# Performance work log

Hardware: AMD Instinct MI355X
Metric: run time of the kernel (lower is better)

Reference implementation:

```python
import jax, jax.numpy as jnp
import numpy as np

CLASSES = [20, 70, 250, 800, 3000, 12000]
DIM = 768
B = 2048


def setup_inputs() -> dict:
    key = jax.random.key(0)
    ks = jax.random.split(key, 2 * len(CLASSES) + 1)
    inp = {"x": jax.random.normal(ks[0], (B, DIM), jnp.float32)}
    scale = 1.0 / np.sqrt(DIM).astype(np.float32)
    for i, c in enumerate(CLASSES):
        # Concatenation of all per-node generator Linear layers at level i.
        inp[f"W{i}"] = jax.random.normal(ks[1 + i], (c, DIM), jnp.float32) * scale
        inp[f"b{i}"] = jnp.zeros((c,), jnp.float32)
    for lvl in range(1, 6):
        k = jax.random.fold_in(key, 100 + lvl)
        # parent index (at level lvl-1) of each class at level lvl; sorted -> contiguous sibling groups
        inp[f"p{lvl}"] = jnp.sort(
            jax.random.randint(k, (CLASSES[lvl],), 0, CLASSES[lvl - 1], jnp.int32)
        )
    return inp


def _segment_softmax_cols(logits, parent, num_parents):
    """Softmax over columns of logits [B, C], within groups of columns sharing a parent."""
    lt = logits.T  # [C, B]
    mx = jax.ops.segment_max(lt, parent, num_segments=num_parents)  # [P, B]
    e = jnp.exp(lt - mx[parent])
    s = jax.ops.segment_sum(e, parent, num_segments=num_parents)  # [P, B]
    return (e / s[parent]).T  # [B, C]


def reference(x, W0, b0, W1, b1, W2, b2, W3, b3, W4, b4, W5, b5, p1, p2, p3, p4, p5):
    # Level 0: root generator = Linear + Softmax over all level-0 classes.
    out = jax.nn.softmax(x @ W0.T + b0, axis=1)  # [B, classes[0]]
    outputs = [out]
    Ws = [W1, W2, W3, W4, W5]
    bs = [b1, b2, b3, b4, b5]
    ps = [p1, p2, p3, p4, p5]
    for lvl in range(5):
        logits = x @ Ws[lvl].T + bs[lvl]  # [B, classes[lvl+1]]
        cond = _segment_softmax_cols(logits, ps[lvl], CLASSES[lvl])  # per-parent softmax
        out = cond * outputs[-1][:, ps[lvl]]  # scatter of prob * subtree(x) == gather of parent prob
        outputs.append(out)
    return tuple(outputs)
```

## Files before the change

### kernel.cpp

```cpp
#include <hip/hip_runtime.h>
#include <stdint.h>

#define BDIM 2048
#define KDIM 768
#define NTOT 16140
#define NKT 24

typedef _Float16 half8 __attribute__((ext_vector_type(8)));
typedef float floatx4 __attribute__((ext_vector_type(4)));

__device__ __forceinline__ unsigned short f2h(float f) {
  _Float16 h = (_Float16)f;
  return __builtin_bit_cast(unsigned short, h);
}

__device__ __forceinline__ void level_of(int col, int& cb, int& Cl, long long& ob) {
  if      (col < 20)   { cb = 0;    Cl = 20;    ob = 0LL; }
  else if (col < 90)   { cb = 20;   Cl = 70;    ob = 40960LL; }
  else if (col < 340)  { cb = 90;   Cl = 250;   ob = 184320LL; }
  else if (col < 1140) { cb = 340;  Cl = 800;   ob = 696320LL; }
  else if (col < 4140) { cb = 1140; Cl = 3000;  ob = 2334720LL; }
  else                 { cb = 4140; Cl = 12000; ob = 8478720LL; }
}

__device__ __forceinline__ void gload_lds16(const void* g, void* l) {
  __builtin_amdgcn_global_load_lds(
      (const __attribute__((address_space(1))) unsigned int*)g,
      (__attribute__((address_space(3))) unsigned int*)l, 16, 0, 0);
}

__global__ __launch_bounds__(256) void convert_kernel(
    const float* __restrict__ x,
    const float* __restrict__ W0, const float* __restrict__ W1,
    const float* __restrict__ W2, const float* __restrict__ W3,
    const float* __restrict__ W4, const float* __restrict__ W5,
    unsigned short* __restrict__ xh, unsigned short* __restrict__ wh)
{
  long long i4 = (long long)blockIdx.x * 256 + threadIdx.x;
  if (i4 >= 3492096LL) return;
  long long e = i4 * 4;
  const long long XN = (long long)BDIM * KDIM;
  float4 v;
  unsigned short* dst;
  if (e < XN) {
    v = reinterpret_cast<const float4*>(x)[i4];
    dst = xh + e;
  } else {
    long long we = e - XN;
    const float* src; long long off;
    if      (we < 15360)    { src = W0; off = we; }
    else if (we < 69120)    { src = W1; off = we - 15360; }
    else if (we < 261120)   { src = W2; off = we - 69120; }
    else if (we < 875520)   { src = W3; off = we - 261120; }
    else if (we < 3179520)  { src = W4; off = we - 875520; }
    else                    { src = W5; off = we - 3179520; }
    v = reinterpret_cast<const float4*>(src)[off >> 2];
    dst = wh + we;
  }
  ushort4 o;
  o.x = f2h(v.x); o.y = f2h(v.y); o.z = f2h(v.z); o.w = f2h(v.w);
  *reinterpret_cast<ushort4*>(dst) = o;
}

__global__ __launch_bounds__(256) void seg_build_kernel(
    const int* __restrict__ p1, const int* __restrict__ p2, const int* __restrict__ p3,
    const int* __restrict__ p4, const int* __restrict__ p5, int* __restrict__ seg)
{
  int idx = blockIdx.x * 256 + threadIdx.x;
  if (idx >= 4147) return;
  int L, s;
  if      (idx < 2)    { L = 0; s = idx; }
  else if (idx < 23)   { L = 1; s = idx - 2; }
  else if (idx < 94)   { L = 2; s = idx - 23; }
  else if (idx < 345)  { L = 3; s = idx - 94; }
  else if (idx < 1146) { L = 4; s = idx - 345; }
  else                 { L = 5; s = idx - 1146; }
  int val;
  if (L == 0) {
    val = (s == 0) ? 0 : 20;
  } else {
    const int* p = (L == 1) ? p1 : (L == 2) ? p2 : (L == 3) ? p3 : (L == 4) ? p4 : p5;
    int C = (L == 1) ? 70 : (L == 2) ? 250 : (L == 3) ? 800 : (L == 4) ? 3000 : 12000;
    int lo = 0, hi = C;
    while (lo < hi) { int mid = (lo + hi) >> 1; if (p[mid] < s) lo = mid + 1; else hi = mid; }
    val = lo;
  }
  seg[idx] = val;
}

#define EPI_STRIDE 132

__global__ __launch_bounds__(256, 2) void gemm_kernel(
    const unsigned short* __restrict__ Ah,
    const unsigned short* __restrict__ Wh,
    float* __restrict__ out)
{
  __shared__ __align__(16) char smem_raw[64 * EPI_STRIDE * 4];
  float* epi = (float*)smem_raw;

  const int bid = blockIdx.x;
  const int logical = (bid & 7) * 254 + (bid >> 3);
  const int cx = logical >> 4;
  const int row0 = (logical & 15) * 128;
  const int col0 = cx * 128;

  const int tid  = threadIdx.x;
  const int wave = tid >> 6;
  const int lane = tid & 63;
  const int wr = (wave >> 1) * 64;
  const int wc = (wave & 1) * 64;
  const int q  = lane >> 4;
  const int lr = lane & 15;

  const int rquad = lane >> 2;
  const int kq = lane & 3;

  floatx4 acc[4][4];
#pragma unroll
  for (int i = 0; i < 4; ++i)
#pragma unroll
    for (int j = 0; j < 4; ++j)
      acc[i][j] = (floatx4){0.f, 0.f, 0.f, 0.f};

  const unsigned short* gA[2];
  const unsigned short* gB[2];
#pragma unroll
  for (int i = 0; i < 2; ++i) {
    int c = 2 * wave + i;
    int rowA = row0 + 16 * c + rquad;
    gA[i] = Ah + (long long)rowA * KDIM + kq * 8;
    int colB = col0 + 16 * c + rquad;
    if (colB >= NTOT) colB = NTOT - 1;
    gB[i] = Wh + (long long)colB * KDIM + kq * 8;
  }

  auto stage = [&](int buf, int kt) {
#pragma unroll
    for (int i = 0; i < 2; ++i) {
      int c = 2 * wave + i;
      gload_lds16(gA[i] + kt * 32, smem_raw + buf * 8192 + c * 1024);
      gload_lds16(gB[i] + kt * 32, smem_raw + 16384 + buf * 8192 + c * 1024);
    }
  };

  int cur = 0;
  stage(0, 0);
  __syncthreads();

  for (int kt = 0; kt < NKT; ++kt) {
    if (kt + 1 < NKT) stage(cur ^ 1, kt + 1);
    const char* Ac = smem_raw + cur * 8192;
    const char* Bc = smem_raw + 16384 + cur * 8192;
    half8 af[4], bf[4];
#pragma unroll
    for (int i = 0; i < 4; ++i)
      af[i] = __builtin_bit_cast(half8, *(const uint4*)(Ac + (wr + i * 16 + lr) * 64 + q * 16));
#pragma unroll
    for (int j = 0; j < 4; ++j)
      bf[j] = __builtin_bit_cast(half8, *(const uint4*)(Bc + (wc + j * 16 + lr) * 64 + q * 16));
#pragma unroll
    for (int i = 0; i < 4; ++i)
#pragma unroll
      for (int j = 0; j < 4; ++j)
        acc[i][j] = __builtin_amdgcn_mfma_f32_16x16x32_f16(af[i], bf[j], acc[i][j], 0, 0, 0);
    __syncthreads();
    cur ^= 1;
  }

  int cbA, ClA; long long obA; level_of(col0, cbA, ClA, obA);
  int cbB, ClB; long long obB; level_of(col0 + 127, cbB, ClB, obB);
  const bool fast = (cbA == cbB) && ((cbA & 3) == 0) && ((ClA & 3) == 0) && (col0 + 128 <= NTOT);

  for (int h = 0; h < 2; ++h) {
    __syncthreads();
    if ((wave >> 1) == h) {
#pragma unroll
      for (int i = 0; i < 4; ++i)
#pragma unroll
        for (int j = 0; j < 4; ++j)
#pragma unroll
          for (int rg = 0; rg < 4; ++rg)
            epi[(i * 16 + q * 4 + rg) * EPI_STRIDE + wc + j * 16 + lr] = acc[i][j][rg];
    }
    __syncthreads();
    if (fast) {
      const long long rowbase = obA + (long long)(row0 + h * 64) * ClA + (col0 - cbA);
#pragma unroll
      for (int it = 0; it < 8; ++it) {
        int idx = it * 256 + tid;
        int r = idx >> 5, f4 = idx & 31;
        float4 v = *(const float4*)(epi + r * EPI_STRIDE + f4 * 4);
        *(float4*)(out + rowbase + (long long)r * ClA + f4 * 4) = v;
      }
    } else {
      for (int idx = tid; idx < 64 * 128; idx += 256) {
        int r = idx >> 7, c = idx & 127;
        int col = col0 + c;
        if (col < NTOT) {
          int cb, Cl; long long ob; level_of(col, cb, Cl, ob);
          out[ob + (long long)(row0 + h * 64 + r) * Cl + (col - cb)] = epi[r * EPI_STRIDE + c];
        }
      }
    }
  }
}

__global__ __launch_bounds__(512) void tree_softmax_kernel(
    float* __restrict__ out,
    const float* __restrict__ b0, const float* __restrict__ b1, const float* __restrict__ b2,
    const float* __restrict__ b3, const float* __restrict__ b4, const float* __restrict__ b5,
    const int* __restrict__ seg,
    const int* __restrict__ p1, const int* __restrict__ p2, const int* __restrict__ p3,
    const int* __restrict__ p4, const int* __restrict__ p5)
{
  __shared__ __align__(16) float l[NTOT];
  __shared__ float rs[3000];
  const int tid = threadIdx.x;
  const int row = blockIdx.x;
  const float* bias[6] = {b0, b1, b2, b3, b4, b5};
  const int* par[6] = {nullptr, p1, p2, p3, p4, p5};
  const int Cn[6] = {20, 70, 250, 800, 3000, 12000};
  const int Pn[6] = {1, 20, 70, 250, 800, 3000};
  const int lb[6] = {0, 20, 90, 340, 1140, 4140};
  const int so[6] = {0, 2, 23, 94, 345, 1146};
  const long long ob[6] = {0, 40960, 184320, 696320, 2334720, 8478720};

#pragma unroll
  for (int L = 0; L < 6; ++L) {
    const float* src = out + ob[L] + (long long)row * Cn[L];
    const float* bs = bias[L];
    float* dst = l + lb[L];
    if ((Cn[L] & 3) == 0 && (lb[L] & 3) == 0) {
      const int n4 = Cn[L] >> 2;
      for (int i = tid; i < n4; i += 512) {
        float4 v = reinterpret_cast<const float4*>(src)[i];
        float4 b = reinterpret_cast<const float4*>(bs)[i];
        float4 e;
        e.x = __expf(v.x + b.x); e.y = __expf(v.y + b.y);
        e.z = __expf(v.z + b.z); e.w = __expf(v.w + b.w);
        reinterpret_cast<float4*>(dst)[i] = e;
      }
    } else {
      for (int c = tid; c < Cn[L]; c += 512) dst[c] = __expf(src[c] + bs[c]);
    }
  }
  __syncthreads();

#pragma unroll
  for (int L = 0; L < 6; ++L) {
    const int* sg = seg + so[L];
    float* lv = l + lb[L];
    const float* pv = l + ((L == 0) ? 0 : lb[L - 1]);
    for (int s = tid; s < Pn[L]; s += 512) {
      int st = sg[s], en = sg[s + 1];
      float sum = 0.f;
      for (int c = st; c < en; ++c) sum += lv[c];
      float pp = (L == 0) ? 1.0f : pv[s];
      rs[s] = pp / sum;
    }
    __syncthreads();
    float* dstg = out + ob[L] + (long long)row * Cn[L];
    if (L == 0) {
      float r0 = rs[0];
      for (int c = tid; c < 20; c += 512) { float v = lv[c] * r0; lv[c] = v; dstg[c] = v; }
    } else if ((Cn[L] & 3) == 0 && (lb[L] & 3) == 0) {
      const int* pa = par[L];
      const int n4 = Cn[L] >> 2;
      for (int i = tid; i < n4; i += 512) {
        int4 pi = reinterpret_cast<const int4*>(pa)[i];
        float4 v = reinterpret_cast<const float4*>(lv)[i];
        v.x *= rs[pi.x]; v.y *= rs[pi.y]; v.z *= rs[pi.z]; v.w *= rs[pi.w];
        if (L != 5) reinterpret_cast<float4*>(lv)[i] = v;
        reinterpret_cast<float4*>(dstg)[i] = v;
      }
    } else {
      const int* pa = par[L];
      for (int c = tid; c < Cn[L]; c += 512) {
        float v = lv[c] * rs[pa[c]];
        lv[c] = v; dstg[c] = v;
      }
    }
    __syncthreads();
  }
}

extern "C" void kernel_launch(void* const* d_in, const int* in_sizes, int n_in,
                              void* d_out, int out_size, void* d_ws, size_t ws_size,
                              hipStream_t stream)
{
  const float* x = (const float*)d_in[0];
  const float* W[6]    = {(const float*)d_in[1], (const float*)d_in[3], (const float*)d_in[5],
                          (const float*)d_in[7], (const float*)d_in[9], (const float*)d_in[11]};
  const float* bias[6] = {(const float*)d_in[2], (const float*)d_in[4], (const float*)d_in[6],
                          (const float*)d_in[8], (const float*)d_in[10], (const float*)d_in[12]};
  const int* p[5] = {(const int*)d_in[13], (const int*)d_in[14], (const int*)d_in[15],
                     (const int*)d_in[16], (const int*)d_in[17]};
  float* out = (float*)d_out;
  char* ws = (char*)d_ws;
  unsigned short* xh = (unsigned short*)ws;
  unsigned short* wh = (unsigned short*)(ws + 3145728);
  int* seg = (int*)(ws + 27936768);

  convert_kernel<<<13641, 256, 0, stream>>>(x, W[0], W[1], W[2], W[3], W[4], W[5], xh, wh);
  seg_build_kernel<<<17, 256, 0, stream>>>(p[0], p[1], p[2], p[3], p[4], seg);
  gemm_kernel<<<2032, 256, 0, stream>>>(xh, wh, out);
  tree_softmax_kernel<<<2048, 512, 0, stream>>>(
      out, bias[0], bias[1], bias[2], bias[3], bias[4], bias[5], seg,
      p[0], p[1], p[2], p[3], p[4]);
}
```

Measured before the change: 367.2 us.

## Replace segment-offset tree softmax with LDS atomic sums and register-held leaves

Measured after the change: 454.4 us. 23.8% more time.

```diff
diff --git a/kernel.cpp b/kernel.cpp
--- a/kernel.cpp
+++ b/kernel.cpp
@@ -62,32 +62,6 @@
   *reinterpret_cast<ushort4*>(dst) = o;
 }
 
-__global__ __launch_bounds__(256) void seg_build_kernel(
-    const int* __restrict__ p1, const int* __restrict__ p2, const int* __restrict__ p3,
-    const int* __restrict__ p4, const int* __restrict__ p5, int* __restrict__ seg)
-{
-  int idx = blockIdx.x * 256 + threadIdx.x;
-  if (idx >= 4147) return;
-  int L, s;
-  if      (idx < 2)    { L = 0; s = idx; }
-  else if (idx < 23)   { L = 1; s = idx - 2; }
-  else if (idx < 94)   { L = 2; s = idx - 23; }
-  else if (idx < 345)  { L = 3; s = idx - 94; }
-  else if (idx < 1146) { L = 4; s = idx - 345; }
-  else                 { L = 5; s = idx - 1146; }
-  int val;
-  if (L == 0) {
-    val = (s == 0) ? 0 : 20;
-  } else {
-    const int* p = (L == 1) ? p1 : (L == 2) ? p2 : (L == 3) ? p3 : (L == 4) ? p4 : p5;
-    int C = (L == 1) ? 70 : (L == 2) ? 250 : (L == 3) ? 800 : (L == 4) ? 3000 : 12000;
-    int lo = 0, hi = C;
-    while (lo < hi) { int mid = (lo + hi) >> 1; if (p[mid] < s) lo = mid + 1; else hi = mid; }
-    val = lo;
-  }
-  seg[idx] = val;
-}
-
 #define EPI_STRIDE 132
 
 __global__ __launch_bounds__(256, 2) void gemm_kernel(
@@ -205,82 +179,121 @@
   }
 }
 
-__global__ __launch_bounds__(512) void tree_softmax_kernel(
+__global__ __launch_bounds__(512, 6) void tree_softmax_kernel(
     float* __restrict__ out,
     const float* __restrict__ b0, const float* __restrict__ b1, const float* __restrict__ b2,
     const float* __restrict__ b3, const float* __restrict__ b4, const float* __restrict__ b5,
-    const int* __restrict__ seg,
     const int* __restrict__ p1, const int* __restrict__ p2, const int* __restrict__ p3,
     const int* __restrict__ p4, const int* __restrict__ p5)
 {
-  __shared__ __align__(16) float l[NTOT];
-  __shared__ float rs[3000];
+  __shared__ float e04[4140];
+  __shared__ float S[4141];
   const int tid = threadIdx.x;
-  const int row = blockIdx.x;
-  const float* bias[6] = {b0, b1, b2, b3, b4, b5};
-  const int* par[6] = {nullptr, p1, p2, p3, p4, p5};
-  const int Cn[6] = {20, 70, 250, 800, 3000, 12000};
-  const int Pn[6] = {1, 20, 70, 250, 800, 3000};
-  const int lb[6] = {0, 20, 90, 340, 1140, 4140};
-  const int so[6] = {0, 2, 23, 94, 345, 1146};
-  const long long ob[6] = {0, 40960, 184320, 696320, 2334720, 8478720};
-
-#pragma unroll
-  for (int L = 0; L < 6; ++L) {
-    const float* src = out + ob[L] + (long long)row * Cn[L];
-    const float* bs = bias[L];
-    float* dst = l + lb[L];
-    if ((Cn[L] & 3) == 0 && (lb[L] & 3) == 0) {
-      const int n4 = Cn[L] >> 2;
-      for (int i = tid; i < n4; i += 512) {
-        float4 v = reinterpret_cast<const float4*>(src)[i];
-        float4 b = reinterpret_cast<const float4*>(bs)[i];
-        float4 e;
-        e.x = __expf(v.x + b.x); e.y = __expf(v.y + b.y);
-        e.z = __expf(v.z + b.z); e.w = __expf(v.w + b.w);
-        reinterpret_cast<float4*>(dst)[i] = e;
-      }
-    } else {
-      for (int c = tid; c < Cn[L]; c += 512) dst[c] = __expf(src[c] + bs[c]);
-    }
-  }
-  __syncthreads();
-
-#pragma unroll
-  for (int L = 0; L < 6; ++L) {
-    const int* sg = seg + so[L];
-    float* lv = l + lb[L];
-    const float* pv = l + ((L == 0) ? 0 : lb[L - 1]);
-    for (int s = tid; s < Pn[L]; s += 512) {
-      int st = sg[s], en = sg[s + 1];
-      float sum = 0.f;
-      for (int c = st; c < en; ++c) sum += lv[c];
-      float pp = (L == 0) ? 1.0f : pv[s];
-      rs[s] = pp / sum;
-    }
-    __syncthreads();
-    float* dstg = out + ob[L] + (long long)row * Cn[L];
-    if (L == 0) {
-      float r0 = rs[0];
-      for (int c = tid; c < 20; c += 512) { float v = lv[c] * r0; lv[c] = v; dstg[c] = v; }
-    } else if ((Cn[L] & 3) == 0 && (lb[L] & 3) == 0) {
-      const int* pa = par[L];
-      const int n4 = Cn[L] >> 2;
-      for (int i = tid; i < n4; i += 512) {
-        int4 pi = reinterpret_cast<const int4*>(pa)[i];
-        float4 v = reinterpret_cast<const float4*>(lv)[i];
-        v.x *= rs[pi.x]; v.y *= rs[pi.y]; v.z *= rs[pi.z]; v.w *= rs[pi.w];
-        if (L != 5) reinterpret_cast<float4*>(lv)[i] = v;
-        reinterpret_cast<float4*>(dstg)[i] = v;
-      }
-    } else {
-      const int* pa = par[L];
-      for (int c = tid; c < Cn[L]; c += 512) {
-        float v = lv[c] * rs[pa[c]];
-        lv[c] = v; dstg[c] = v;
-      }
-    }
-    __syncthreads();
+  const long long row = blockIdx.x;
+
+  for (int i = tid; i < 4141; i += 512) S[i] = 0.f;
+  __syncthreads();
+
+  if (tid < 20) {
+    float e = __expf(out[row * 20 + tid] + b0[tid]);
+    e04[tid] = e;
+    atomicAdd(&S[0], e);
+  }
+  if (tid < 70) {
+    float e = __expf(out[40960 + row * 70 + tid] + b1[tid]);
+    e04[20 + tid] = e;
+    atomicAdd(&S[1 + p1[tid]], e);
+  }
+  if (tid < 250) {
+    float e = __expf(out[184320 + row * 250 + tid] + b2[tid]);
+    e04[90 + tid] = e;
+    atomicAdd(&S[21 + p2[tid]], e);
+  }
+  if (tid < 200) {
+    float4 v = reinterpret_cast<const float4*>(out + 696320 + row * 800)[tid];
+    float4 b = reinterpret_cast<const float4*>(b3)[tid];
+    int4  p = reinterpret_cast<const int4*>(p3)[tid];
+    float4 e;
+    e.x = __expf(v.x + b.x); e.y = __expf(v.y + b.y);
+    e.z = __expf(v.z + b.z); e.w = __expf(v.w + b.w);
+    reinterpret_cast<float4*>(e04 + 340)[tid] = e;
+    atomicAdd(&S[91 + p.x], e.x); atomicAdd(&S[91 + p.y], e.y);
+    atomicAdd(&S[91 + p.z], e.z); atomicAdd(&S[91 + p.w], e.w);
+  }
+  for (int i4 = tid; i4 < 750; i4 += 512) {
+    float4 v = reinterpret_cast<const float4*>(out + 2334720 + row * 3000)[i4];
+    float4 b = reinterpret_cast<const float4*>(b4)[i4];
+    int4  p = reinterpret_cast<const int4*>(p4)[i4];
+    float4 e;
+    e.x = __expf(v.x + b.x); e.y = __expf(v.y + b.y);
+    e.z = __expf(v.z + b.z); e.w = __expf(v.w + b.w);
+    reinterpret_cast<float4*>(e04 + 1140)[i4] = e;
+    atomicAdd(&S[341 + p.x], e.x); atomicAdd(&S[341 + p.y], e.y);
+    atomicAdd(&S[341 + p.z], e.z); atomicAdd(&S[341 + p.w], e.w);
+  }
+  float4 e5[6];
+  const float4* l5 = reinterpret_cast<const float4*>(out + 8478720 + row * 12000);
+  const float4* b5v = reinterpret_cast<const float4*>(b5);
+  const int4*  p5v = reinterpret_cast<const int4*>(p5);
+#pragma unroll
+  for (int i = 0; i < 6; ++i) {
+    int i4 = i * 512 + tid;
+    if (i4 < 3000) {
+      float4 v = l5[i4]; float4 b = b5v[i4]; int4 p = p5v[i4];
+      float4 e;
+      e.x = __expf(v.x + b.x); e.y = __expf(v.y + b.y);
+      e.z = __expf(v.z + b.z); e.w = __expf(v.w + b.w);
+      e5[i] = e;
+      atomicAdd(&S[1141 + p.x], e.x); atomicAdd(&S[1141 + p.y], e.y);
+      atomicAdd(&S[1141 + p.z], e.z); atomicAdd(&S[1141 + p.w], e.w);
+    }
+  }
+  __syncthreads();
+
+  if (tid == 0) S[0] = 1.f / S[0];
+  __syncthreads();
+  if (tid < 20)  S[1 + tid]  = e04[tid]       * S[0]            / S[1 + tid];
+  __syncthreads();
+  if (tid < 70)  S[21 + tid] = e04[20 + tid]  * S[1 + p1[tid]]  / S[21 + tid];
+  __syncthreads();
+  if (tid < 250) S[91 + tid] = e04[90 + tid]  * S[21 + p2[tid]] / S[91 + tid];
+  __syncthreads();
+  for (int s = tid; s < 800; s += 512)
+    S[341 + s]  = e04[340 + s]  * S[91 + p3[s]]  / S[341 + s];
+  __syncthreads();
+  for (int s = tid; s < 3000; s += 512)
+    S[1141 + s] = e04[1140 + s] * S[341 + p4[s]] / S[1141 + s];
+  __syncthreads();
+
+  if (tid < 20)
+    out[row * 20 + tid] = e04[tid] * S[0];
+  if (tid < 70)
+    out[40960 + row * 70 + tid] = e04[20 + tid] * S[1 + p1[tid]];
+  if (tid < 250)
+    out[184320 + row * 250 + tid] = e04[90 + tid] * S[21 + p2[tid]];
+  if (tid < 200) {
+    int4 p = reinterpret_cast<const int4*>(p3)[tid];
+    float4 e = reinterpret_cast<const float4*>(e04 + 340)[tid];
+    e.x *= S[91 + p.x]; e.y *= S[91 + p.y]; e.z *= S[91 + p.z]; e.w *= S[91 + p.w];
+    reinterpret_cast<float4*>(out + 696320 + row * 800)[tid] = e;
+  }
+  for (int i4 = tid; i4 < 750; i4 += 512) {
+    int4 p = reinterpret_cast<const int4*>(p4)[i4];
+    float4 e = reinterpret_cast<const float4*>(e04 + 1140)[i4];
+    e.x *= S[341 + p.x]; e.y *= S[341 + p.y]; e.z *= S[341 + p.z]; e.w *= S[341 + p.w];
+    reinterpret_cast<float4*>(out + 2334720 + row * 3000)[i4] = e;
+  }
+  float4* o5 = reinterpret_cast<float4*>(out + 8478720 + row * 12000);
+#pragma unroll
+  for (int i = 0; i < 6; ++i) {
+    int i4 = i * 512 + tid;
+    if (i4 < 3000) {
+      int4 p = p5v[i4];
+      float4 e = e5[i];
+      e.x *= S[1141 + p.x]; e.y *= S[1141 + p.y];
+      e.z *= S[1141 + p.z]; e.w *= S[1141 + p.w];
+      o5[i4] = e;
+    }
   }
 }
 
@@ -299,12 +312,10 @@
   char* ws = (char*)d_ws;
   unsigned short* xh = (unsigned short*)ws;
   unsigned short* wh = (unsigned short*)(ws + 3145728);
-  int* seg = (int*)(ws + 27936768);
 
   convert_kernel<<<13641, 256, 0, stream>>>(x, W[0], W[1], W[2], W[3], W[4], W[5], xh, wh);
-  seg_build_kernel<<<17, 256, 0, stream>>>(p[0], p[1], p[2], p[3], p[4], seg);
   gemm_kernel<<<2032, 256, 0, stream>>>(xh, wh, out);
   tree_softmax_kernel<<<2048, 512, 0, stream>>>(
-      out, bias[0], bias[1], bias[2], bias[3], bias[4], bias[5], seg,
+      out, bias[0], bias[1], bias[2], bias[3], bias[4], bias[5],
       p[0], p[1], p[2], p[3], p[4]);
 }
```
